# Kernel tuning notes

Measured on AMD Instinct MI355X. Metric: run time of the kernel, lower is better.

## Reference

```python
import jax, jax.numpy as jnp
import numpy as np

LORA_RANK = 16
LORA_ALPHA = 32.0
LORA_SCALE = LORA_ALPHA / LORA_RANK
W_BITS = 8
A_BITS = 8


def fake_quant(x, bits):
    """Symmetric per-tensor fake quantization with straight-through estimator."""
    qmax = 2.0 ** (bits - 1) - 1.0
    scale = jnp.maximum(jnp.max(jnp.abs(x)), 1e-8) / qmax
    q = jnp.clip(jnp.round(x / scale), -qmax, qmax) * scale
    return x + jax.lax.stop_gradient(q - x)  # STE


def quant_linear_lora(x, W, b, A, B):
    # x: [..., in], W: [out, in], A: [r, in], B: [out, r]
    xq = fake_quant(x, A_BITS)
    Wq = fake_quant(W, W_BITS)
    base = jnp.einsum('bsi,oi->bso', xq, Wq) + b
    lora = jnp.einsum('bsr,or->bso', jnp.einsum('bsi,ri->bsr', x, A), B)
    return base + LORA_SCALE * lora


def setup_inputs() -> dict:
    key = jax.random.key(0)
    ks = jax.random.split(key, 9)
    n_embd, d_ff, B_, S = 1024, 4096, 4, 2048
    s_in = 1.0 / np.sqrt(n_embd)
    s_ff = 1.0 / np.sqrt(d_ff)
    return {
        'hidden_states': jax.random.normal(ks[0], (B_, S, n_embd), jnp.float32),
        'W_fc': jax.random.normal(ks[1], (d_ff, n_embd), jnp.float32) * s_in,
        'b_fc': jax.random.normal(ks[2], (d_ff,), jnp.float32) * 0.02,
        'A_fc': jax.random.normal(ks[3], (LORA_RANK, n_embd), jnp.float32) * s_in,
        'B_fc': jax.random.normal(ks[4], (d_ff, LORA_RANK), jnp.float32) * 0.01,
        'W_proj': jax.random.normal(ks[5], (n_embd, d_ff), jnp.float32) * s_ff,
        'b_proj': jax.random.normal(ks[6], (n_embd,), jnp.float32) * 0.02,
        'A_proj': jax.random.normal(ks[7], (LORA_RANK, d_ff), jnp.float32) * s_ff,
        'B_proj': jax.random.normal(ks[8], (n_embd, LORA_RANK), jnp.float32) * 0.01,
    }


def reference(hidden_states, W_fc, b_fc, A_fc, B_fc, W_proj, b_proj, A_proj, B_proj):
    h = quant_linear_lora(hidden_states, W_fc, b_fc, A_fc, B_fc)
    h = jax.nn.gelu(h, approximate=False)  # nn.GELU() default = exact erf GELU
    h = quant_linear_lora(h, W_proj, b_proj, A_proj, B_proj)
    return h
```

## Files before the change

### kernel.cpp

```cpp
#include <hip/hip_runtime.h>
#include <stdint.h>

using i32x4 = __attribute__((ext_vector_type(4))) int;
using f32x4 = __attribute__((ext_vector_type(4))) float;
using f16x4 = __attribute__((ext_vector_type(4))) _Float16;

#define M_TOK 8192
#define N_EMB 1024
#define D_FF  4096

__device__ __forceinline__ void async_lds16(void* lds, const void* g) {
  __builtin_amdgcn_global_load_lds(
      (const __attribute__((address_space(1))) void*)g,
      (__attribute__((address_space(3))) void*)lds, 16, 0, 0);
}

__global__ void zero_slots_k(unsigned* s) {
  if (threadIdx.x < 16) s[threadIdx.x] = 0u;
}

__global__ void absmax3_k(const float* __restrict__ p0, long n0,
                          const float* __restrict__ p1, long n1,
                          const float* __restrict__ p2, long n2,
                          unsigned* __restrict__ slots) {
  const float* p = blockIdx.y == 0 ? p0 : (blockIdx.y == 1 ? p1 : p2);
  long n = blockIdx.y == 0 ? n0 : (blockIdx.y == 1 ? n1 : n2);
  unsigned* slot = slots + blockIdx.y;

  long i = ((long)blockIdx.x * blockDim.x + threadIdx.x) * 4;
  long stride = (long)gridDim.x * blockDim.x * 4;
  float m = 0.f;
  for (; i < n; i += stride) {
    float4 v = *(const float4*)(p + i);
    m = fmaxf(m, fmaxf(fmaxf(fabsf(v.x), fabsf(v.y)), fmaxf(fabsf(v.z), fabsf(v.w))));
  }
  for (int o = 32; o; o >>= 1) m = fmaxf(m, __shfl_xor(m, o));
  __shared__ float sm[4];
  if ((threadIdx.x & 63) == 0) sm[threadIdx.x >> 6] = m;
  __syncthreads();
  if (threadIdx.x == 0) {
    m = fmaxf(fmaxf(sm[0], sm[1]), fmaxf(sm[2], sm[3]));
    atomicMax(slot, __float_as_uint(m));
  }
}

__global__ void quant2_k(const float* __restrict__ p0, int8_t* __restrict__ q0, long n0,
                         const float* __restrict__ p1, int8_t* __restrict__ q1, long n1,
                         const unsigned* __restrict__ slots) {
  const float* p = blockIdx.y == 0 ? p0 : p1;
  int8_t* q = blockIdx.y == 0 ? q0 : q1;
  long n = blockIdx.y == 0 ? n0 : n1;
  float inv = 127.f / fmaxf(__uint_as_float(slots[blockIdx.y + 1]), 1e-8f);

  long i = ((long)blockIdx.x * blockDim.x + threadIdx.x) * 4;
  long stride = (long)gridDim.x * blockDim.x * 4;
  for (; i < n; i += stride) {
    float4 v = *(const float4*)(p + i);
    int b0 = (int)fminf(fmaxf(rintf(v.x * inv), -127.f), 127.f);
    int b1 = (int)fminf(fmaxf(rintf(v.y * inv), -127.f), 127.f);
    int b2 = (int)fminf(fmaxf(rintf(v.z * inv), -127.f), 127.f);
    int b3 = (int)fminf(fmaxf(rintf(v.w * inv), -127.f), 127.f);
    int w = (b0 & 0xff) | ((b1 & 0xff) << 8) | ((b2 & 0xff) << 16) | ((b3 & 0xff) << 24);
    *(int*)(q + i) = w;
  }
}

__global__ void prep_bfrag_k(const float* __restrict__ A, _Float16* __restrict__ Bp, int K) {
  int s = blockIdx.x;
  int l = threadIdx.x;
  int r = l & 15, g = l >> 4;
  float4 v = *(const float4*)(A + (long)r * K + s * 16 + g * 4);
  f16x4 h;
  h[0] = (_Float16)v.x; h[1] = (_Float16)v.y; h[2] = (_Float16)v.z; h[3] = (_Float16)v.w;
  *(f16x4*)(Bp + ((long)s * 64 + l) * 4) = h;
}

__global__ __launch_bounds__(512) void lora_quant_k(
    const float* __restrict__ X, const _Float16* __restrict__ Bpre,
    const unsigned* __restrict__ slot, int8_t* __restrict__ Q,
    float* __restrict__ T, int K) {
  int lane = threadIdx.x & 63, wave = threadIdx.x >> 6;
  int row0 = blockIdx.x * 16;
  int r = lane & 15, g = lane >> 4;
  float inv = 127.f / fmaxf(__uint_as_float(*slot), 1e-8f);

  int kPerWave = K >> 3;
  int kbase = wave * kPerWave;
  const float* xrow = X + (long)(row0 + r) * K;
  int8_t* qrow = Q + (long)(row0 + r) * K;

  f32x4 acc = {0.f, 0.f, 0.f, 0.f};
  int nsteps = kPerWave >> 4;
#pragma unroll 4
  for (int s = 0; s < nsteps; s++) {
    int k = kbase + s * 16 + g * 4;
    float4 v = *(const float4*)(xrow + k);
    int b0 = (int)fminf(fmaxf(rintf(v.x * inv), -127.f), 127.f);
    int b1 = (int)fminf(fmaxf(rintf(v.y * inv), -127.f), 127.f);
    int b2 = (int)fminf(fmaxf(rintf(v.z * inv), -127.f), 127.f);
    int b3 = (int)fminf(fmaxf(rintf(v.w * inv), -127.f), 127.f);
    *(int*)(qrow + k) = (b0 & 0xff) | ((b1 & 0xff) << 8) | ((b2 & 0xff) << 16) | ((b3 & 0xff) << 24);
    f16x4 a;
    a[0] = (_Float16)v.x; a[1] = (_Float16)v.y; a[2] = (_Float16)v.z; a[3] = (_Float16)v.w;
    int gs = (kbase + s * 16) >> 4;
    f16x4 b = *(const f16x4*)(Bpre + ((long)gs * 64 + lane) * 4);
    acc = __builtin_amdgcn_mfma_f32_16x16x16f16(a, b, acc, 0, 0, 0);
  }

  __shared__ float part[8][16][17];
#pragma unroll
  for (int j = 0; j < 4; j++) part[wave][g * 4 + j][r] = acc[j];
  __syncthreads();
  int t = threadIdx.x;
  if (t < 256) {
    int m = t >> 4, rr = t & 15;
    float sum = 0.f;
#pragma unroll
    for (int w = 0; w < 8; w++) sum += part[w][m][rr];
    T[(long)(row0 + m) * 16 + rr] = 2.0f * sum;
  }
}

template <bool GELU, int NF>
__global__ __launch_bounds__(512) void gemm8p(
    const int8_t* __restrict__ Aq, const int8_t* __restrict__ Bq,
    int N, int K,
    const unsigned* __restrict__ sa, const unsigned* __restrict__ sb,
    const float* __restrict__ bias,
    const float* __restrict__ T,
    const float* __restrict__ Bl,
    float* __restrict__ C, unsigned* hmax) {
  constexpr int BN = NF * 64;
  constexpr int BBUF = BN * 128;
  __shared__ __align__(16) int8_t lds[65536 + 2 * BBUF];
  int8_t* ldsA = lds;
  int8_t* ldsB = lds + 65536;

  int nwg = gridDim.x * gridDim.y;
  int lid = blockIdx.y * gridDim.x + blockIdx.x;
  int cpx = nwg >> 3;
  int nid = (lid & 7) * cpx + (lid >> 3);
  int bn = (nid % gridDim.x) * BN;
  int bm = (nid / gridDim.x) * 256;

  int t = threadIdx.x;
  int lane = t & 63, wave = t >> 6;
  int wr = wave >> 2, wc = wave & 3;
  int l16 = lane & 15, lq = lane >> 4;

  const int8_t* gA = Aq + (long)bm * K;
  const int8_t* gB = Bq + (long)bn * K;

  int aDst[4], aSrc[4];
#pragma unroll
  for (int i = 0; i < 4; i++) {
    int s = i * 512 + t, row = s >> 3;
    aDst[i] = s * 16;
    aSrc[i] = row * K + (((s & 7) ^ (row & 7)) << 4);
  }
  int bDst[NF], bSrc[NF];
#pragma unroll
  for (int i = 0; i < NF; i++) {
    int s = i * 512 + t, row = s >> 3;
    bDst[i] = s * 16;
    bSrc[i] = row * K + (((s & 7) ^ (row & 7)) << 4);
  }

  int aoff[8], boff[NF];
#pragma unroll
  for (int mf = 0; mf < 8; mf++) {
    int row = wr * 128 + mf * 16 + l16;
    aoff[mf] = row * 128 + ((lq ^ (row & 7)) << 4);
  }
#pragma unroll
  for (int nf = 0; nf < NF; nf++) {
    int row = wc * (NF * 16) + nf * 16 + l16;
    boff[nf] = row * 128 + ((lq ^ (row & 7)) << 4);
  }

  i32x4 acc[8][NF] = {};
  int KT = K >> 7;

#pragma unroll
  for (int i = 0; i < 4; i++) async_lds16(ldsA + aDst[i], gA + aSrc[i]);
#pragma unroll
  for (int i = 0; i < NF; i++) async_lds16(ldsB + bDst[i], gB + bSrc[i]);
#pragma unroll
  for (int i = 0; i < 4; i++) async_lds16(ldsA + 32768 + aDst[i], gA + aSrc[i] + 128);
  asm volatile("s_waitcnt vmcnt(4)" ::: "memory");
  __builtin_amdgcn_s_barrier();
  __builtin_amdgcn_sched_barrier(0);

  for (int kt = 0; kt < KT; ++kt) {
    const int8_t* Ab = ldsA + (kt & 1) * 32768;
    const int8_t* Bb = ldsB + (kt & 1) * BBUF;

    if (kt + 1 < KT) {
      long ko = (long)(kt + 1) * 128;
      int nb = ((kt + 1) & 1) * BBUF;
#pragma unroll
      for (int i = 0; i < NF; i++) async_lds16(ldsB + nb + bDst[i], gB + bSrc[i] + ko);
    }

#pragma unroll
    for (int ks = 0; ks < 2; ks++) {
      int kx = ks << 6;
      i32x4 av[8], bv[NF];
#pragma unroll
      for (int mf = 0; mf < 8; mf++) av[mf] = *(const i32x4*)(Ab + (aoff[mf] ^ kx));
#pragma unroll
      for (int nf = 0; nf < NF; nf++) bv[nf] = *(const i32x4*)(Bb + (boff[nf] ^ kx));
      __builtin_amdgcn_s_setprio(1);
#pragma unroll
      for (int mf = 0; mf < 8; mf++)
#pragma unroll
        for (int nf = 0; nf < NF; nf++)
          acc[mf][nf] = __builtin_amdgcn_mfma_i32_16x16x64_i8(av[mf], bv[nf], acc[mf][nf], 0, 0, 0);
      __builtin_amdgcn_s_setprio(0);
    }

    __builtin_amdgcn_sched_barrier(0);
    __builtin_amdgcn_s_barrier();
    if (kt + 2 < KT) {
      long ko = (long)(kt + 2) * 128;
      int nb = (kt & 1) * 32768;
#pragma unroll
      for (int i = 0; i < 4; i++) async_lds16(ldsA + nb + aDst[i], gA + aSrc[i] + ko);
      asm volatile("s_waitcnt vmcnt(4)" ::: "memory");
      __builtin_amdgcn_s_barrier();
      __builtin_amdgcn_sched_barrier(0);
    } else if (kt + 1 < KT) {
      asm volatile("s_waitcnt vmcnt(0)" ::: "memory");
      __builtin_amdgcn_s_barrier();
      __builtin_amdgcn_sched_barrier(0);
    }
  }

  float s = (fmaxf(__uint_as_float(*sa), 1e-8f) * (1.f / 127.f)) *
            (fmaxf(__uint_as_float(*sb), 1e-8f) * (1.f / 127.f));

  f16x4 af[8], bf[NF];
#pragma unroll
  for (int mf = 0; mf < 8; mf++) {
    int m = bm + wr * 128 + mf * 16 + l16;
    float4 tv = *(const float4*)(T + (long)m * 16 + lq * 4);
    f16x4 v; v[0] = (_Float16)tv.x; v[1] = (_Float16)tv.y; v[2] = (_Float16)tv.z; v[3] = (_Float16)tv.w;
    af[mf] = v;
  }
#pragma unroll
  for (int nf = 0; nf < NF; nf++) {
    int n = bn + wc * (NF * 16) + nf * 16 + l16;
    float4 bv4 = *(const float4*)(Bl + (long)n * 16 + lq * 4);
    f16x4 v; v[0] = (_Float16)bv4.x; v[1] = (_Float16)bv4.y; v[2] = (_Float16)bv4.z; v[3] = (_Float16)bv4.w;
    bf[nf] = v;
  }
  float bias_v[NF];
#pragma unroll
  for (int nf = 0; nf < NF; nf++) bias_v[nf] = bias[bn + wc * (NF * 16) + nf * 16 + l16];

  float lmax = 0.f;
#pragma unroll
  for (int mf = 0; mf < 8; mf++) {
#pragma unroll
    for (int nf = 0; nf < NF; nf++) {
      f32x4 fa = __builtin_amdgcn_mfma_f32_16x16x16f16(af[mf], bf[nf], f32x4{0.f, 0.f, 0.f, 0.f}, 0, 0, 0);
      int n = bn + wc * (NF * 16) + nf * 16 + l16;
#pragma unroll
      for (int j = 0; j < 4; j++) {
        int m = bm + wr * 128 + mf * 16 + lq * 4 + j;
        float v = s * (float)acc[mf][nf][j] + bias_v[nf] + fa[j];
        if constexpr (GELU) {
          v = 0.5f * v * (1.0f + erff(v * 0.70710678118654752f));
          lmax = fmaxf(lmax, fabsf(v));
        }
        C[(long)m * N + n] = v;
      }
    }
  }
  if constexpr (GELU) {
    for (int o = 32; o; o >>= 1) lmax = fmaxf(lmax, __shfl_xor(lmax, o));
    if (lane == 0) atomicMax(hmax, __float_as_uint(lmax));
  }
}

extern "C" void kernel_launch(void* const* d_in, const int* in_sizes, int n_in,
                              void* d_out, int out_size, void* d_ws, size_t ws_size,
                              hipStream_t stream) {
  const float* x   = (const float*)d_in[0];
  const float* Wfc = (const float*)d_in[1];
  const float* bfc = (const float*)d_in[2];
  const float* Afc = (const float*)d_in[3];
  const float* Bfc = (const float*)d_in[4];
  const float* Wpj = (const float*)d_in[5];
  const float* bpj = (const float*)d_in[6];
  const float* Apj = (const float*)d_in[7];
  const float* Bpj = (const float*)d_in[8];
  float* out = (float*)d_out;

  char* ws = (char*)d_ws;
  unsigned* slots = (unsigned*)ws;
  int8_t* qx  = (int8_t*)(ws + 256);
  int8_t* qwf = qx  + (size_t)M_TOK * N_EMB;
  int8_t* qwp = qwf + (size_t)D_FF * N_EMB;
  int8_t* qh  = qwp + (size_t)N_EMB * D_FF;
  float*  t1  = (float*)(qh + (size_t)M_TOK * D_FF);
  float*  t2  = t1  + (size_t)M_TOK * 16;
  _Float16* Bp1 = (_Float16*)(t2 + (size_t)M_TOK * 16);
  _Float16* Bp2 = Bp1 + (size_t)N_EMB * 16;
  float*  h   = (float*)(Bp2 + (size_t)D_FF * 16);

  zero_slots_k<<<1, 64, 0, stream>>>(slots);

  absmax3_k<<<dim3(1024, 3), 256, 0, stream>>>(
      x, (long)M_TOK * N_EMB, Wfc, (long)D_FF * N_EMB, Wpj, (long)N_EMB * D_FF, slots);

  quant2_k<<<dim3(2048, 2), 256, 0, stream>>>(
      Wfc, qwf, (long)D_FF * N_EMB, Wpj, qwp, (long)N_EMB * D_FF, slots);

  prep_bfrag_k<<<N_EMB / 16, 64, 0, stream>>>(Afc, Bp1, N_EMB);
  prep_bfrag_k<<<D_FF / 16, 64, 0, stream>>>(Apj, Bp2, D_FF);

  lora_quant_k<<<M_TOK / 16, 512, 0, stream>>>(x, Bp1, slots + 0, qx, t1, N_EMB);

  gemm8p<true, 4><<<dim3(D_FF / 256, M_TOK / 256), 512, 0, stream>>>(
      qx, qwf, D_FF, N_EMB, slots + 0, slots + 1, bfc, t1, Bfc, h, slots + 3);

  lora_quant_k<<<M_TOK / 16, 512, 0, stream>>>(h, Bp2, slots + 3, qh, t2, D_FF);

  gemm8p<false, 2><<<dim3(N_EMB / 128, M_TOK / 256), 512, 0, stream>>>(
      qh, qwp, N_EMB, D_FF, slots + 3, slots + 2, bpj, t2, Bpj, out, nullptr);
}
```

Measured before the change: 272.6 us.

## Triple-buffer int8 GEMM LDS pipeline and shrink first GEMM N-tile

Replaces the double-buffered A/B staging in the int8 MFMA GEMM with a three-stage ring buffer. Loads for stage kt+3 are issued after each compute step, with vmcnt waits adjusted to match, so global-to-LDS latency gets more slack. The first GEMM also switches from NF=4 (256-wide N tiles) to NF=2 (128-wide), which doubles its grid and cuts LDS per block to fit the third buffer. The cost is less reuse of each A tile per block, more total A traffic, and higher LDS use (about 144KB per block) that limits occupancy.

```diff
diff --git a/kernel.cpp b/kernel.cpp
--- a/kernel.cpp
+++ b/kernel.cpp
@@ -122,7 +122,7 @@
 }
 
 template <bool GELU, int NF>
-__global__ __launch_bounds__(512) void gemm8p(
+__global__ __launch_bounds__(512) void gemm_d3(
     const int8_t* __restrict__ Aq, const int8_t* __restrict__ Bq,
     int N, int K,
     const unsigned* __restrict__ sa, const unsigned* __restrict__ sb,
@@ -131,10 +131,12 @@
     const float* __restrict__ Bl,
     float* __restrict__ C, unsigned* hmax) {
   constexpr int BN = NF * 64;
+  constexpr int ABUF = 32768;
   constexpr int BBUF = BN * 128;
-  __shared__ __align__(16) int8_t lds[65536 + 2 * BBUF];
+  constexpr int BL = BBUF / 16 / 512;
+  __shared__ __align__(16) int8_t lds[3 * ABUF + 3 * BBUF];
   int8_t* ldsA = lds;
-  int8_t* ldsB = lds + 65536;
+  int8_t* ldsB = lds + 3 * ABUF;
 
   int nwg = gridDim.x * gridDim.y;
   int lid = blockIdx.y * gridDim.x + blockIdx.x;
@@ -158,9 +160,9 @@
     aDst[i] = s * 16;
     aSrc[i] = row * K + (((s & 7) ^ (row & 7)) << 4);
   }
-  int bDst[NF], bSrc[NF];
-#pragma unroll
-  for (int i = 0; i < NF; i++) {
+  int bDst[BL], bSrc[BL];
+#pragma unroll
+  for (int i = 0; i < BL; i++) {
     int s = i * 512 + t, row = s >> 3;
     bDst[i] = s * 16;
     bSrc[i] = row * K + (((s & 7) ^ (row & 7)) << 4);
@@ -181,26 +183,26 @@
   i32x4 acc[8][NF] = {};
   int KT = K >> 7;
 
-#pragma unroll
-  for (int i = 0; i < 4; i++) async_lds16(ldsA + aDst[i], gA + aSrc[i]);
-#pragma unroll
-  for (int i = 0; i < NF; i++) async_lds16(ldsB + bDst[i], gB + bSrc[i]);
-#pragma unroll
-  for (int i = 0; i < 4; i++) async_lds16(ldsA + 32768 + aDst[i], gA + aSrc[i] + 128);
-  asm volatile("s_waitcnt vmcnt(4)" ::: "memory");
+  auto issue = [&](int g) {
+    long ko = (long)g * 128;
+    int8_t* ab = ldsA + (g % 3) * ABUF;
+    int8_t* bb = ldsB + (g % 3) * BBUF;
+#pragma unroll
+    for (int i = 0; i < 4; i++) async_lds16(ab + aDst[i], gA + aSrc[i] + ko);
+#pragma unroll
+    for (int i = 0; i < BL; i++) async_lds16(bb + bDst[i], gB + bSrc[i] + ko);
+  };
+
+  issue(0);
+  issue(1);
+  issue(2);
+  asm volatile("s_waitcnt vmcnt(12)" ::: "memory");
   __builtin_amdgcn_s_barrier();
   __builtin_amdgcn_sched_barrier(0);
 
   for (int kt = 0; kt < KT; ++kt) {
-    const int8_t* Ab = ldsA + (kt & 1) * 32768;
-    const int8_t* Bb = ldsB + (kt & 1) * BBUF;
-
-    if (kt + 1 < KT) {
-      long ko = (long)(kt + 1) * 128;
-      int nb = ((kt + 1) & 1) * BBUF;
-#pragma unroll
-      for (int i = 0; i < NF; i++) async_lds16(ldsB + nb + bDst[i], gB + bSrc[i] + ko);
-    }
+    const int8_t* Ab = ldsA + (kt % 3) * ABUF;
+    const int8_t* Bb = ldsB + (kt % 3) * BBUF;
 
 #pragma unroll
     for (int ks = 0; ks < 2; ks++) {
@@ -221,16 +223,16 @@
 
     __builtin_amdgcn_sched_barrier(0);
     __builtin_amdgcn_s_barrier();
-    if (kt + 2 < KT) {
-      long ko = (long)(kt + 2) * 128;
-      int nb = (kt & 1) * 32768;
-#pragma unroll
-      for (int i = 0; i < 4; i++) async_lds16(ldsA + nb + aDst[i], gA + aSrc[i] + ko);
-      asm volatile("s_waitcnt vmcnt(4)" ::: "memory");
-      __builtin_amdgcn_s_barrier();
-      __builtin_amdgcn_sched_barrier(0);
-    } else if (kt + 1 < KT) {
-      asm volatile("s_waitcnt vmcnt(0)" ::: "memory");
+
+    if (kt + 3 < KT) issue(kt + 3);
+    if (kt + 1 < KT) {
+      if (kt + 3 < KT) {
+        asm volatile("s_waitcnt vmcnt(12)" ::: "memory");
+      } else if (kt + 2 < KT) {
+        asm volatile("s_waitcnt vmcnt(6)" ::: "memory");
+      } else {
+        asm volatile("s_waitcnt vmcnt(0)" ::: "memory");
+      }
       __builtin_amdgcn_s_barrier();
       __builtin_amdgcn_sched_barrier(0);
     }
@@ -322,11 +324,11 @@
 
   lora_quant_k<<<M_TOK / 16, 512, 0, stream>>>(x, Bp1, slots + 0, qx, t1, N_EMB);
 
-  gemm8p<true, 4><<<dim3(D_FF / 256, M_TOK / 256), 512, 0, stream>>>(
+  gemm_d3<true, 2><<<dim3(D_FF / 128, M_TOK / 256), 512, 0, stream>>>(
       qx, qwf, D_FF, N_EMB, slots + 0, slots + 1, bfc, t1, Bfc, h, slots + 3);
 
   lora_quant_k<<<M_TOK / 16, 512, 0, stream>>>(h, Bp2, slots + 3, qh, t2, D_FF);
 
-  gemm8p<false, 2><<<dim3(N_EMB / 128, M_TOK / 256), 512, 0, stream>>>(
+  gemm_d3<false, 2><<<dim3(N_EMB / 128, M_TOK / 256), 512, 0, stream>>>(
       qh, qwp, N_EMB, D_FF, slots + 3, slots + 2, bpj, t2, Bpj, out, nullptr);
 }
```

Result: slower. 313.4 us (+15.0%).
